# Kernel tuning notes

Measured on AMD Instinct MI355X. Metric: run time of the kernel, lower is better.

The kernel has to match this reference:

```python
import jax, jax.numpy as jnp
import numpy as np

B, L, D, E = 32, 2048, 1024, 2048

def setup_inputs() -> dict:
    key = jax.random.key(0)
    k1, k2, k3, k4, k5 = jax.random.split(key, 5)
    scale_s = 1.0 / np.sqrt(D)
    scale_h = 1.0 / np.sqrt(E)
    return {
        "dec_hidden": jax.random.normal(k1, (B, D), jnp.float32),
        "enc_outputs": jax.random.normal(k2, (B, L, E), jnp.float32),
        "W_s": jax.random.normal(k3, (D, D), jnp.float32) * scale_s,
        "W_h": jax.random.normal(k4, (D, E), jnp.float32) * scale_h,
        "v": jax.random.normal(k5, (D,), jnp.float32) * scale_s,
    }

def reference(dec_hidden, enc_outputs, W_s, W_h, v):
    # s: [B, D] -- projected decoder state (broadcast over src_len, no repeat)
    s = jnp.einsum('bd,ed->be', dec_hidden, W_s)
    # h: [B, L, D] -- projected encoder outputs
    h = jnp.einsum('ble,de->bld', enc_outputs, W_h)
    # additive scores: v^T tanh(s + h) -> [B, L]
    scores = jnp.einsum('bld,d->bl', jnp.tanh(s[:, None, :] + h), v)
    attn = jax.nn.softmax(scores, axis=1)
    # context: weighted sum of encoder outputs -> [B, E]
    ctx = jnp.einsum('bl,ble->be', attn, enc_outputs)
    return (ctx, attn)
```

## Files before the change

### kernel.cpp

```cpp
#include <hip/hip_runtime.h>
#include <cstdint>
#include <cstddef>

#define B_ 32
#define L_ 2048
#define D_ 1024
#define E_ 2048

typedef __attribute__((ext_vector_type(8))) short short8;
typedef __attribute__((ext_vector_type(4))) float f32x4;
typedef __attribute__((ext_vector_type(4))) unsigned int uint4v;

__device__ __forceinline__ void async_copy16(const void* g, void* l) {
  __builtin_amdgcn_global_load_lds((const __attribute__((address_space(1))) void*)g,
                                   (__attribute__((address_space(3))) void*)l, 16, 0, 0);
}

__device__ __forceinline__ unsigned int pack_bf16_2(float lo, float hi) {
  unsigned int ul = __builtin_bit_cast(unsigned int, lo) + 0x8000u;
  unsigned int uh = __builtin_bit_cast(unsigned int, hi) + 0x8000u;
  return (ul >> 16) | (uh & 0xFFFF0000u);
}

__device__ __forceinline__ float fast_tanh(float x) {
  float e = __expf(2.0f * x);
  return 1.0f - 2.0f / (e + 1.0f);
}

__global__ __launch_bounds__(256) void k_s(const float* __restrict__ dec,
                                           const float* __restrict__ Ws,
                                           float* __restrict__ s) {
  int wid = threadIdx.x >> 6, lane = threadIdx.x & 63;
  int out = blockIdx.x * 4 + wid;
  int b = out >> 10, i = out & 1023;
  const float* dr = dec + b * D_;
  const float* wr = Ws + (size_t)i * D_;
  float acc = 0.f;
#pragma unroll
  for (int c = 0; c < 4; ++c) {
    int d0 = c * 256 + lane * 4;
    float4 x = *(const float4*)(dr + d0);
    float4 w = *(const float4*)(wr + d0);
    acc += x.x * w.x + x.y * w.y + x.z * w.z + x.w * w.w;
  }
#pragma unroll
  for (int off = 32; off >= 1; off >>= 1) acc += __shfl_xor(acc, off, 64);
  if (lane == 0) s[out] = acc;
}

__global__ __launch_bounds__(256) void k_cvt(const float* __restrict__ src,
                                             unsigned short* __restrict__ dst) {
  size_t i = ((size_t)blockIdx.x * 256 + threadIdx.x) * 8;
  float4 a = *(const float4*)(src + i);
  float4 b = *(const float4*)(src + i + 4);
  uint4v p;
  p.x = pack_bf16_2(a.x, a.y);
  p.y = pack_bf16_2(a.z, a.w);
  p.z = pack_bf16_2(b.x, b.y);
  p.w = pack_bf16_2(b.z, b.w);
  *(uint4v*)(dst + i) = p;
}

__global__ __launch_bounds__(256) void k_gemm(const float* __restrict__ enc,
                                              const unsigned short* __restrict__ whb,
                                              const float* __restrict__ sbias,
                                              const float* __restrict__ vvec,
                                              float* __restrict__ scores) {
  __shared__ alignas(16) float As[128 * 32];
  __shared__ alignas(16) unsigned short Bs[128 * 32];

  const int tid = threadIdx.x;
  const int wid = tid >> 6;
  const int lane = tid & 63;

  const int flat = blockIdx.x;
  const int nt = (flat >> 3) & 7;
  const int mt = (flat & 7) | ((flat >> 6) << 3);
  const int m_base = mt * 128, n_base = nt * 128;
  const int b_idx = m_base >> 11;

  const int aRow = wid * 32 + (lane >> 3);
  const int aCol = (((lane & 7) ^ ((lane >> 3) & 7)) << 2);
  const float* gA = enc + (size_t)(m_base + aRow) * E_ + aCol;
  const int bRow = wid * 32 + (lane >> 2);
  const int bCol = (((lane & 3) ^ ((lane >> 3) & 3)) << 3);
  const unsigned short* gB = whb + (size_t)(n_base + bRow) * E_ + bCol;

  float* ldsA = &As[wid * 1024];
  unsigned short* ldsB = &Bs[wid * 1024];

  const int waveM = wid & 1, waveN = wid >> 1;
  const int mrow = waveM * 64 + (lane & 15);
  const int nrow = waveN * 64 + (lane & 15);

  const float* aptr0[4];
  const float* aptr1[4];
  const unsigned short* bptr[4];
  {
    const int g0 = (lane >> 4) * 2;
    const int gb = (lane >> 4);
#pragma unroll
    for (int mi = 0; mi < 4; ++mi) {
      int rl = mrow + mi * 16;
      aptr0[mi] = &As[rl * 32 + (((g0) ^ (rl & 7)) << 2)];
      aptr1[mi] = &As[rl * 32 + (((g0 + 1) ^ (rl & 7)) << 2)];
    }
#pragma unroll
    for (int ni = 0; ni < 4; ++ni) {
      int rl = nrow + ni * 16;
      bptr[ni] = &Bs[rl * 32 + ((gb ^ ((rl >> 1) & 3)) << 3)];
    }
  }

  f32x4 acc[4][4] = {};

  for (int kk = 0; kk < E_; kk += 32) {
    __syncthreads();
#pragma unroll
    for (int it = 0; it < 4; ++it)
      async_copy16(gA + (size_t)(it * 8) * E_ + kk, ldsA + it * 256);
#pragma unroll
    for (int it = 0; it < 2; ++it)
      async_copy16(gB + (size_t)(it * 16) * E_ + kk, ldsB + it * 512);
    __syncthreads();

    short8 bf[4];
#pragma unroll
    for (int ni = 0; ni < 4; ++ni) bf[ni] = *(const short8*)bptr[ni];
#pragma unroll
    for (int mi = 0; mi < 4; ++mi) {
      float4 f0 = *(const float4*)aptr0[mi];
      float4 f1 = *(const float4*)aptr1[mi];
      uint4v pa;
      pa.x = pack_bf16_2(f0.x, f0.y);
      pa.y = pack_bf16_2(f0.z, f0.w);
      pa.z = pack_bf16_2(f1.x, f1.y);
      pa.w = pack_bf16_2(f1.z, f1.w);
      short8 af = __builtin_bit_cast(short8, pa);
#pragma unroll
      for (int ni = 0; ni < 4; ++ni)
        acc[mi][ni] = __builtin_amdgcn_mfma_f32_16x16x32_bf16(af, bf[ni], acc[mi][ni], 0, 0, 0);
    }
  }

  float vv[4], sv[4];
#pragma unroll
  for (int ni = 0; ni < 4; ++ni) {
    int n = n_base + nrow + ni * 16;
    vv[ni] = vvec[n];
    sv[ni] = sbias[b_idx * D_ + n];
  }
  const int quad = lane >> 4;
#pragma unroll
  for (int mi = 0; mi < 4; ++mi) {
#pragma unroll
    for (int r = 0; r < 4; ++r) {
      float sum = 0.f;
#pragma unroll
      for (int ni = 0; ni < 4; ++ni)
        sum += vv[ni] * fast_tanh(sv[ni] + acc[mi][ni][r]);
      sum += __shfl_xor(sum, 1, 16);
      sum += __shfl_xor(sum, 2, 16);
      sum += __shfl_xor(sum, 4, 16);
      sum += __shfl_xor(sum, 8, 16);
      if ((lane & 15) == 0)
        atomicAdd(&scores[m_base + waveM * 64 + mi * 16 + quad * 4 + r], sum);
    }
  }
}

__global__ __launch_bounds__(256) void k_softmax(float* __restrict__ sc) {
  int b = blockIdx.x, tid = threadIdx.x;
  int lane = tid & 63, wid = tid >> 6;
  float* row = sc + (size_t)b * L_;
  float vals[8];
  float mx = -1e30f;
#pragma unroll
  for (int j = 0; j < 8; ++j) { vals[j] = row[tid + j * 256]; mx = fmaxf(mx, vals[j]); }
#pragma unroll
  for (int off = 32; off >= 1; off >>= 1) mx = fmaxf(mx, __shfl_xor(mx, off, 64));
  __shared__ float redm[4], reds[4];
  if (lane == 0) redm[wid] = mx;
  __syncthreads();
  mx = fmaxf(fmaxf(redm[0], redm[1]), fmaxf(redm[2], redm[3]));
  float sum = 0.f;
#pragma unroll
  for (int j = 0; j < 8; ++j) { vals[j] = __expf(vals[j] - mx); sum += vals[j]; }
#pragma unroll
  for (int off = 32; off >= 1; off >>= 1) sum += __shfl_xor(sum, off, 64);
  if (lane == 0) reds[wid] = sum;
  __syncthreads();
  sum = reds[0] + reds[1] + reds[2] + reds[3];
  float inv = 1.0f / sum;
#pragma unroll
  for (int j = 0; j < 8; ++j) row[tid + j * 256] = vals[j] * inv;
}

__global__ __launch_bounds__(256) void k_ctx(const float* __restrict__ enc,
                                             const float* __restrict__ attn,
                                             float* __restrict__ ctx) {
  int b = blockIdx.y, lc = blockIdx.x;
  int t = threadIdx.x;
  __shared__ float aw[128];
  if (t < 128) aw[t] = attn[(size_t)b * L_ + lc * 128 + t];
  __syncthreads();
  const float* base = enc + ((size_t)b * L_ + (size_t)lc * 128) * E_;
  float4 a0 = make_float4(0.f, 0.f, 0.f, 0.f);
  float4 a1 = make_float4(0.f, 0.f, 0.f, 0.f);
#pragma unroll 2
  for (int l = 0; l < 128; ++l) {
    float w = aw[l];
    const float* r = base + (size_t)l * E_;
    float4 x0 = *(const float4*)(r + t * 4);
    float4 x1 = *(const float4*)(r + 1024 + t * 4);
    a0.x += w * x0.x; a0.y += w * x0.y; a0.z += w * x0.z; a0.w += w * x0.w;
    a1.x += w * x1.x; a1.y += w * x1.y; a1.z += w * x1.z; a1.w += w * x1.w;
  }
  float* cb = ctx + (size_t)b * E_;
  atomicAdd(cb + t * 4 + 0, a0.x);
  atomicAdd(cb + t * 4 + 1, a0.y);
  atomicAdd(cb + t * 4 + 2, a0.z);
  atomicAdd(cb + t * 4 + 3, a0.w);
  atomicAdd(cb + 1024 + t * 4 + 0, a1.x);
  atomicAdd(cb + 1024 + t * 4 + 1, a1.y);
  atomicAdd(cb + 1024 + t * 4 + 2, a1.z);
  atomicAdd(cb + 1024 + t * 4 + 3, a1.w);
}

extern "C" void kernel_launch(void* const* d_in, const int* in_sizes, int n_in,
                              void* d_out, int out_size, void* d_ws, size_t ws_size,
                              hipStream_t stream) {
  const float* dec = (const float*)d_in[0];
  const float* enc = (const float*)d_in[1];
  const float* Ws  = (const float*)d_in[2];
  const float* Wh  = (const float*)d_in[3];
  const float* v   = (const float*)d_in[4];

  float* ctx  = (float*)d_out;
  float* attn = (float*)d_out + B_ * E_;

  unsigned short* whb = (unsigned short*)d_ws;
  float* sbuf = (float*)((char*)d_ws + (size_t)D_ * E_ * sizeof(unsigned short));

  hipMemsetAsync(d_out, 0, (size_t)out_size * sizeof(float), stream);

  k_s<<<dim3((B_ * D_) / 4), dim3(256), 0, stream>>>(dec, Ws, sbuf);
  k_cvt<<<dim3((D_ * E_) / (256 * 8)), dim3(256), 0, stream>>>(Wh, whb);
  k_gemm<<<dim3((B_ * L_ / 128) * (D_ / 128)), dim3(256), 0, stream>>>(enc, whb, sbuf, v, attn);
  k_softmax<<<dim3(B_), dim3(256), 0, stream>>>(attn);
  k_ctx<<<dim3(L_ / 128, B_), dim3(256), 0, stream>>>(enc, attn, ctx);
}
```

Measured before the change: 1.184 ms.

## Switch score GEMM to 32x32x16 MFMA with two-wave 128x128 tiles

Rewrites the fused score GEMM to use 32x32x16 bf16 MFMA instructions with 128-thread blocks, where each of two waves computes a 64x128 sub-tile. It also drops the grouped block-index swizzle in favor of a simple row-major tile order. The aim is to get more MFMA work per LDS read and fewer instructions per FLOP. In exchange, each wave holds more accumulator registers and has fewer waves to hide latency, the simpler tile order may reduce L2 reuse, and the tanh/v epilogue reduction now spans 32 lanes.

Result: slower. 1.243 ms (+5.0%).

```diff
diff --git a/kernel.cpp b/kernel.cpp
--- a/kernel.cpp
+++ b/kernel.cpp
@@ -8,7 +8,7 @@
 #define E_ 2048
 
 typedef __attribute__((ext_vector_type(8))) short short8;
-typedef __attribute__((ext_vector_type(4))) float f32x4;
+typedef __attribute__((ext_vector_type(16))) float f32x16;
 typedef __attribute__((ext_vector_type(4))) unsigned int uint4v;
 
 __device__ __forceinline__ void async_copy16(const void* g, void* l) {
@@ -61,11 +61,11 @@
   *(uint4v*)(dst + i) = p;
 }
 
-__global__ __launch_bounds__(256) void k_gemm(const float* __restrict__ enc,
-                                              const unsigned short* __restrict__ whb,
-                                              const float* __restrict__ sbias,
-                                              const float* __restrict__ vvec,
-                                              float* __restrict__ scores) {
+__global__ __launch_bounds__(128, 2) void k_gemm(const float* __restrict__ enc,
+                                                 const unsigned short* __restrict__ whb,
+                                                 const float* __restrict__ sbias,
+                                                 const float* __restrict__ vvec,
+                                                 float* __restrict__ scores) {
   __shared__ alignas(16) float As[128 * 32];
   __shared__ alignas(16) unsigned short Bs[128 * 32];
 
@@ -74,97 +74,98 @@
   const int lane = tid & 63;
 
   const int flat = blockIdx.x;
-  const int nt = (flat >> 3) & 7;
-  const int mt = (flat & 7) | ((flat >> 6) << 3);
+  const int nt = flat & 7;
+  const int mt = flat >> 3;
   const int m_base = mt * 128, n_base = nt * 128;
   const int b_idx = m_base >> 11;
 
-  const int aRow = wid * 32 + (lane >> 3);
-  const int aCol = (((lane & 7) ^ ((lane >> 3) & 7)) << 2);
-  const float* gA = enc + (size_t)(m_base + aRow) * E_ + aCol;
-  const int bRow = wid * 32 + (lane >> 2);
-  const int bCol = (((lane & 3) ^ ((lane >> 3) & 3)) << 3);
-  const unsigned short* gB = whb + (size_t)(n_base + bRow) * E_ + bCol;
-
-  float* ldsA = &As[wid * 1024];
-  unsigned short* ldsB = &Bs[wid * 1024];
-
-  const int waveM = wid & 1, waveN = wid >> 1;
-  const int mrow = waveM * 64 + (lane & 15);
-  const int nrow = waveN * 64 + (lane & 15);
-
-  const float* aptr0[4];
-  const float* aptr1[4];
-  const unsigned short* bptr[4];
-  {
-    const int g0 = (lane >> 4) * 2;
-    const int gb = (lane >> 4);
-#pragma unroll
-    for (int mi = 0; mi < 4; ++mi) {
-      int rl = mrow + mi * 16;
-      aptr0[mi] = &As[rl * 32 + (((g0) ^ (rl & 7)) << 2)];
-      aptr1[mi] = &As[rl * 32 + (((g0 + 1) ^ (rl & 7)) << 2)];
+  const int aRowL = lane >> 3;
+  const int aColF = ((lane & 7) ^ (aRowL & 7)) * 4;
+  const int bRowL = lane >> 2;
+  const int bColH = ((lane & 3) ^ (bRowL & 3)) * 8;
+
+  const float* gA = enc + (size_t)(m_base + wid * 64 + aRowL) * E_ + aColF;
+  const unsigned short* gB = whb + (size_t)(n_base + wid * 64 + bRowL) * E_ + bColH;
+
+  const int col = lane & 31;
+  const int h = lane >> 5;
+  const unsigned short* bptr[4][2];
+#pragma unroll
+  for (int ni = 0; ni < 4; ++ni)
+#pragma unroll
+    for (int ks = 0; ks < 2; ++ks) {
+      int r = ni * 32 + col;
+      int u = ks * 2 + h;
+      bptr[ni][ks] = &Bs[r * 32 + ((u ^ (r & 3)) * 8)];
     }
-#pragma unroll
-    for (int ni = 0; ni < 4; ++ni) {
-      int rl = nrow + ni * 16;
-      bptr[ni] = &Bs[rl * 32 + ((gb ^ ((rl >> 1) & 3)) << 3)];
-    }
-  }
-
-  f32x4 acc[4][4] = {};
+  const float* aptr[2][2][2];
+#pragma unroll
+  for (int mi = 0; mi < 2; ++mi)
+#pragma unroll
+    for (int ks = 0; ks < 2; ++ks)
+#pragma unroll
+      for (int j = 0; j < 2; ++j) {
+        int r = wid * 64 + mi * 32 + col;
+        int u = ks * 4 + h * 2 + j;
+        aptr[mi][ks][j] = &As[r * 32 + ((u ^ (r & 7)) * 4)];
+      }
+
+  f32x16 acc[2][4] = {};
 
   for (int kk = 0; kk < E_; kk += 32) {
     __syncthreads();
 #pragma unroll
+    for (int it = 0; it < 8; ++it)
+      async_copy16(gA + (size_t)(it * 8) * E_ + kk, &As[(wid * 64 + it * 8) * 32]);
+#pragma unroll
     for (int it = 0; it < 4; ++it)
-      async_copy16(gA + (size_t)(it * 8) * E_ + kk, ldsA + it * 256);
-#pragma unroll
-    for (int it = 0; it < 2; ++it)
-      async_copy16(gB + (size_t)(it * 16) * E_ + kk, ldsB + it * 512);
+      async_copy16(gB + (size_t)(it * 16) * E_ + kk, &Bs[(wid * 64 + it * 16) * 32]);
     __syncthreads();
 
-    short8 bf[4];
-#pragma unroll
-    for (int ni = 0; ni < 4; ++ni) bf[ni] = *(const short8*)bptr[ni];
-#pragma unroll
-    for (int mi = 0; mi < 4; ++mi) {
-      float4 f0 = *(const float4*)aptr0[mi];
-      float4 f1 = *(const float4*)aptr1[mi];
-      uint4v pa;
-      pa.x = pack_bf16_2(f0.x, f0.y);
-      pa.y = pack_bf16_2(f0.z, f0.w);
-      pa.z = pack_bf16_2(f1.x, f1.y);
-      pa.w = pack_bf16_2(f1.z, f1.w);
-      short8 af = __builtin_bit_cast(short8, pa);
-#pragma unroll
-      for (int ni = 0; ni < 4; ++ni)
-        acc[mi][ni] = __builtin_amdgcn_mfma_f32_16x16x32_bf16(af, bf[ni], acc[mi][ni], 0, 0, 0);
+#pragma unroll
+    for (int ks = 0; ks < 2; ++ks) {
+      short8 bf[4];
+#pragma unroll
+      for (int ni = 0; ni < 4; ++ni) bf[ni] = *(const short8*)bptr[ni][ks];
+#pragma unroll
+      for (int mi = 0; mi < 2; ++mi) {
+        float4 f0 = *(const float4*)aptr[mi][ks][0];
+        float4 f1 = *(const float4*)aptr[mi][ks][1];
+        uint4v pa;
+        pa.x = pack_bf16_2(f0.x, f0.y);
+        pa.y = pack_bf16_2(f0.z, f0.w);
+        pa.z = pack_bf16_2(f1.x, f1.y);
+        pa.w = pack_bf16_2(f1.z, f1.w);
+        short8 af = __builtin_bit_cast(short8, pa);
+#pragma unroll
+        for (int ni = 0; ni < 4; ++ni)
+          acc[mi][ni] = __builtin_amdgcn_mfma_f32_32x32x16_bf16(af, bf[ni], acc[mi][ni], 0, 0, 0);
+      }
     }
   }
 
   float vv[4], sv[4];
 #pragma unroll
   for (int ni = 0; ni < 4; ++ni) {
-    int n = n_base + nrow + ni * 16;
+    int n = n_base + ni * 32 + col;
     vv[ni] = vvec[n];
     sv[ni] = sbias[b_idx * D_ + n];
   }
-  const int quad = lane >> 4;
-#pragma unroll
-  for (int mi = 0; mi < 4; ++mi) {
-#pragma unroll
-    for (int r = 0; r < 4; ++r) {
+#pragma unroll
+  for (int mi = 0; mi < 2; ++mi) {
+#pragma unroll
+    for (int reg = 0; reg < 16; ++reg) {
       float sum = 0.f;
 #pragma unroll
       for (int ni = 0; ni < 4; ++ni)
-        sum += vv[ni] * fast_tanh(sv[ni] + acc[mi][ni][r]);
-      sum += __shfl_xor(sum, 1, 16);
-      sum += __shfl_xor(sum, 2, 16);
-      sum += __shfl_xor(sum, 4, 16);
-      sum += __shfl_xor(sum, 8, 16);
-      if ((lane & 15) == 0)
-        atomicAdd(&scores[m_base + waveM * 64 + mi * 16 + quad * 4 + r], sum);
+        sum += vv[ni] * fast_tanh(sv[ni] + acc[mi][ni][reg]);
+      sum += __shfl_xor(sum, 1, 64);
+      sum += __shfl_xor(sum, 2, 64);
+      sum += __shfl_xor(sum, 4, 64);
+      sum += __shfl_xor(sum, 8, 64);
+      sum += __shfl_xor(sum, 16, 64);
+      if (col == 0)
+        atomicAdd(&scores[m_base + wid * 64 + mi * 32 + (reg & 3) + 8 * (reg >> 2) + h * 4], sum);
     }
   }
 }
@@ -246,7 +247,7 @@
 
   k_s<<<dim3((B_ * D_) / 4), dim3(256), 0, stream>>>(dec, Ws, sbuf);
   k_cvt<<<dim3((D_ * E_) / (256 * 8)), dim3(256), 0, stream>>>(Wh, whb);
-  k_gemm<<<dim3((B_ * L_ / 128) * (D_ / 128)), dim3(256), 0, stream>>>(enc, whb, sbuf, v, attn);
+  k_gemm<<<dim3((B_ * L_ / 128) * (D_ / 128)), dim3(128), 0, stream>>>(enc, whb, sbuf, v, attn);
   k_softmax<<<dim3(B_), dim3(256), 0, stream>>>(attn);
   k_ctx<<<dim3(L_ / 128, B_), dim3(256), 0, stream>>>(enc, attn, ctx);
 }
```
